# Kernel tuning notes

Measured on AMD Instinct MI355X. Metric: run time of the kernel, lower is better.

Reference implementation:

```python
import jax, jax.numpy as jnp
import numpy as np

TASK_WEIGHT = 1.0
PHYSICS_WEIGHT = 0.3
HZ = 50.0


def physics_scores(w, hz=HZ):
    """Vectorized port of _score_window_raw. w: [B, T, 3] float. Assumes T >= 20.
    Returns float32 [B] scores in {0, 55..90}."""
    w = jax.lax.stop_gradient(w)  # torch version detaches via .cpu().item()
    B, T, _ = w.shape
    n = T
    mean = jnp.mean(w, axis=1, keepdims=True)          # [B,1,3]
    d = w - mean                                        # centered
    tv = jnp.sum(d * d, axis=(1, 2)) / n                # [B] total (biased) variance
    reject = tv < 0.005
    # per-axis saturation check: too many samples pinned at max |value|
    absw = jnp.abs(w)                                   # [B,T,3]
    max_val = jnp.max(absw, axis=1)                     # [B,3]
    at_max_frac = jnp.mean(jnp.abs(absw - max_val[:, None, :]) < 0.01, axis=1)  # [B,3]
    reject |= jnp.any((max_val >= 0.5) & (at_max_frac > 0.2), axis=1)
    # jerk law (hz >= 50): central-difference twice, p95 of |jerk| pooled over axes
    if hz >= 50:
        dt = 1.0 / hz
        vel = (w[:, 2:, :] - w[:, :-2, :]) / (2 * dt)       # [B, T-2, 3]
        jerk = (vel[:, 2:, :] - vel[:, :-2, :]) / (2 * dt)  # [B, T-4, 3]
        jerks = jnp.abs(jerk).reshape(B, -1)                # [B, 3*(T-4)]
        js = jnp.sort(jerks, axis=1)
        p95_idx = int(jerks.shape[1] * 0.95)                # matches jerks[int(len*0.95)]
        reject |= js[:, p95_idx] > 5000
    # variance-tier score
    s1 = jnp.where(tv > 10.0, 90.0,
         jnp.where(tv > 2.0, 80.0,
         jnp.where(tv > 0.5, 70.0, 58.0)))
    # zero-crossing rate of centered x-axis
    dx = d[:, :, 0]                                      # [B,T]
    zcr = jnp.sum(dx[:, 1:] * dx[:, :-1] < 0, axis=1) / n
    s2 = jnp.where(zcr > 0.15, 85.0, jnp.where(zcr > 0.07, 70.0, 55.0))
    score = jnp.floor((s1 + s2) / 2.0)                   # int() truncation (values positive)
    return jnp.where(reject, 0.0, score).astype(jnp.float32)


def setup_inputs() -> dict:
    key = jax.random.key(0)
    k1, k2, k3 = jax.random.split(key, 3)
    B, T, C = 32768, 512, 128
    predictions = jax.random.normal(k1, (B, C), dtype=jnp.float32)
    labels = jax.random.randint(k2, (B,), 0, C, dtype=jnp.int64)
    # scale accel so physics checks pass with realistic-looking noise (std 0.1 m/s^2)
    imu_windows = 0.1 * jax.random.normal(k3, (B, T, 3), dtype=jnp.float32)
    return {"predictions": predictions, "labels": labels, "imu_windows": imu_windows}


def reference(predictions, labels, imu_windows):
    # task loss: mean cross-entropy
    logp = jax.nn.log_softmax(predictions, axis=-1)                      # [B,C]
    task_loss = -jnp.mean(jnp.take_along_axis(logp, labels[:, None], axis=1)[:, 0])
    # physics penalty
    scores = physics_scores(imu_windows, HZ)                             # [B]
    physics_penalty = jnp.mean(1.0 - scores / 100.0)
    return TASK_WEIGHT * task_loss + PHYSICS_WEIGHT * physics_penalty
```

## Files before the change

### kernel.cpp

```cpp
#include <hip/hip_runtime.h>
#include <math.h>

template <int CTRL>
__device__ __forceinline__ float dpp_zero_f(float x) {
    return __int_as_float(__builtin_amdgcn_update_dpp(
        0, __float_as_int(x), CTRL, 0xf, 0xf, true));
}
template <int CTRL>
__device__ __forceinline__ float dpp_self_f(float x) {
    return __int_as_float(__builtin_amdgcn_update_dpp(
        __float_as_int(x), __float_as_int(x), CTRL, 0xf, 0xf, false));
}
template <int CTRL>
__device__ __forceinline__ int dpp_zero_i(int x) {
    return __builtin_amdgcn_update_dpp(0, x, CTRL, 0xf, 0xf, true);
}

__device__ __forceinline__ float dpp_sum_f(float x) {
    x += dpp_zero_f<0x111>(x);
    x += dpp_zero_f<0x112>(x);
    x += dpp_zero_f<0x114>(x);
    x += dpp_zero_f<0x118>(x);
    x += dpp_zero_f<0x142>(x);
    x += dpp_zero_f<0x143>(x);
    return __int_as_float(__builtin_amdgcn_readlane(__float_as_int(x), 63));
}
__device__ __forceinline__ float dpp_max_f(float x) {
    x = fmaxf(x, dpp_self_f<0x111>(x));
    x = fmaxf(x, dpp_self_f<0x112>(x));
    x = fmaxf(x, dpp_self_f<0x114>(x));
    x = fmaxf(x, dpp_self_f<0x118>(x));
    x = fmaxf(x, dpp_self_f<0x142>(x));
    x = fmaxf(x, dpp_self_f<0x143>(x));
    return __int_as_float(__builtin_amdgcn_readlane(__float_as_int(x), 63));
}
__device__ __forceinline__ int dpp_sum_i(int x) {
    x += dpp_zero_i<0x111>(x);
    x += dpp_zero_i<0x112>(x);
    x += dpp_zero_i<0x114>(x);
    x += dpp_zero_i<0x118>(x);
    x += dpp_zero_i<0x142>(x);
    x += dpp_zero_i<0x143>(x);
    return __builtin_amdgcn_readlane(x, 63);
}

template <int CT_T, int CT_C>
__global__ void fused_kernel(const float* __restrict__ imu,
                             const float* __restrict__ preds,
                             const int* __restrict__ labels,
                             float* __restrict__ taskP,
                             float* __restrict__ scoreP,
                             int B, int T_rt, int C_rt) {
    extern __shared__ float lds[];
    __shared__ float shT[4], shS[4];
    const int wave = threadIdx.x >> 6, lane = threadIdx.x & 63;
    const int row = blockIdx.x * 4 + wave;
    const int T = (CT_T > 0) ? CT_T : T_rt;
    const int N = T * 3;
    float* L = lds + wave * N;
    const bool active = (row < B);

    if (active) {
        const float4* src4 = (const float4*)(imu + (size_t)row * (size_t)N);
        float4* dst4 = (float4*)L;
        const int n4 = N >> 2;
        for (int i = lane; i < n4; i += 64) dst4[i] = src4[i];
    }

    float loss = 0.f;
    if (active) {
        const int C = (CT_C > 0) ? CT_C : C_rt;
        constexpr int NV = (CT_C > 0) ? (CT_C / 64) : 16;
        const int nv = (CT_C > 0) ? NV : ((C_rt + 63) >> 6);
        const float* x = preds + (size_t)row * (size_t)C;
        float vals[NV];
        float m = -3.4e38f;
#pragma unroll
        for (int i = 0; i < NV; i++) {
            if (CT_C == 0 && i >= nv) break;
            const int c = lane + (i << 6);
            float v = (CT_C > 0 || c < C) ? x[c] : -3.4e38f;
            vals[i] = v;
            m = fmaxf(m, v);
        }
        m = dpp_max_f(m);
        float s = 0.f;
#pragma unroll
        for (int i = 0; i < NV; i++) {
            if (CT_C == 0 && i >= nv) break;
            const int c = lane + (i << 6);
            if (CT_C > 0 || c < C) s += expf(vals[i] - m);
        }
        s = dpp_sum_f(s);
        const int label = labels[row];
        const int src = label & 63, idx = label >> 6;
        float cand = vals[0];
#pragma unroll
        for (int i = 1; i < NV; i++) {
            if (CT_C == 0 && i >= nv) break;
            if (i == idx) cand = vals[i];
        }
        float xl = __shfl(cand, src, 64);
        loss = logf(s) + m - xl;
    }
    __syncthreads();

    float score = 0.f;
    if (active) {
        constexpr int KMAX = (CT_T > 0) ? (CT_T + 63) / 64 : 16;
        const int kmax = (CT_T > 0) ? KMAX : ((T_rt + 63) >> 6);
        float v0[KMAX], v1[KMAX], v2[KMAX];
        float sum0 = 0, sum1 = 0, sum2 = 0, sq = 0;
        float mx0 = 0, mx1 = 0, mx2 = 0;
        int jerkcnt = 0;
#pragma unroll
        for (int k = 0; k < KMAX; k++) {
            if (CT_T == 0 && k >= kmax) break;
            const int t = lane + (k << 6);
            float a = 0, b = 0, c = 0;
            if (CT_T > 0 || t < T) { a = L[t * 3 + 0]; b = L[t * 3 + 1]; c = L[t * 3 + 2]; }
            v0[k] = a; v1[k] = b; v2[k] = c;
            sum0 += a; sum1 += b; sum2 += c;
            sq += a * a + b * b + c * c;
            mx0 = fmaxf(mx0, fabsf(a));
            mx1 = fmaxf(mx1, fabsf(b));
            mx2 = fmaxf(mx2, fabsf(c));
            if (t < T - 4) {
                float a2 = L[(t + 2) * 3 + 0], b2 = L[(t + 2) * 3 + 1], c2 = L[(t + 2) * 3 + 2];
                float a4 = L[(t + 4) * 3 + 0], b4 = L[(t + 4) * 3 + 1], c4 = L[(t + 4) * 3 + 2];
                jerkcnt += (fabsf(625.f * (a4 - 2.f * a2 + a)) > 5000.f);
                jerkcnt += (fabsf(625.f * (b4 - 2.f * b2 + b)) > 5000.f);
                jerkcnt += (fabsf(625.f * (c4 - 2.f * c2 + c)) > 5000.f);
            }
        }
        sum0 = dpp_sum_f(sum0);
        sum1 = dpp_sum_f(sum1);
        sum2 = dpp_sum_f(sum2);
        sq   = dpp_sum_f(sq);
        mx0  = dpp_max_f(mx0);
        mx1  = dpp_max_f(mx1);
        mx2  = dpp_max_f(mx2);
        const float n = (float)T;
        const float m0 = sum0 / n;
        const float tv = (sq - (sum0 * sum0 + sum1 * sum1 + sum2 * sum2) / n) / n;

        int a0 = 0, a1 = 0, a2c = 0, zc = 0;
#pragma unroll
        for (int k = 0; k < KMAX; k++) {
            if (CT_T == 0 && k >= kmax) break;
            const int t = lane + (k << 6);
            if (CT_T > 0 || t < T) {
                a0  += (fabsf(fabsf(v0[k]) - mx0) < 0.01f);
                a1  += (fabsf(fabsf(v1[k]) - mx1) < 0.01f);
                a2c += (fabsf(fabsf(v2[k]) - mx2) < 0.01f);
                if (t < T - 1) {
                    float dxt = v0[k] - m0;
                    float dxn = L[(t + 1) * 3 + 0] - m0;
                    zc += (dxt * dxn < 0.f);
                }
            }
        }
        int pk1 = a0 | (a1 << 10) | (a2c << 20);
        int pk2 = zc | (jerkcnt << 16);
        pk1 = dpp_sum_i(pk1);
        pk2 = dpp_sum_i(pk2);
        a0 = pk1 & 1023; a1 = (pk1 >> 10) & 1023; a2c = (pk1 >> 20) & 1023;
        zc = pk2 & 0xffff; jerkcnt = pk2 >> 16;

        bool reject = (tv < 0.005f);
        const float fT = (float)T;
        if (mx0 >= 0.5f && (a0  / fT) > 0.2f) reject = true;
        if (mx1 >= 0.5f && (a1  / fT) > 0.2f) reject = true;
        if (mx2 >= 0.5f && (a2c / fT) > 0.2f) reject = true;
        const int jtot = (T - 4) * 3;
        const int p95 = (int)((double)jtot * 0.95);
        if (jerkcnt >= jtot - p95) reject = true;

        const float s1 = tv > 10.f ? 90.f : (tv > 2.f ? 80.f : (tv > 0.5f ? 70.f : 58.f));
        const float zcr = zc / fT;
        const float s2 = zcr > 0.15f ? 85.f : (zcr > 0.07f ? 70.f : 55.f);
        score = floorf((s1 + s2) * 0.5f);
        if (reject) score = 0.f;
    }

    if (lane == 0) { shT[wave] = loss; shS[wave] = score; }
    __syncthreads();
    if (threadIdx.x == 0) {
        taskP[blockIdx.x]  = shT[0] + shT[1] + shT[2] + shT[3];
        scoreP[blockIdx.x] = shS[0] + shS[1] + shS[2] + shS[3];
    }
}

__device__ __forceinline__ float wave_reduce_sum_shfl(float v) {
#pragma unroll
    for (int off = 32; off > 0; off >>= 1) v += __shfl_xor(v, off, 64);
    return v;
}

__global__ void finalize_kernel(const float* __restrict__ p1, const float* __restrict__ p2,
                                int n1, int n2, float* __restrict__ out, int B) {
    __shared__ float sh1[4], sh2[4];
    const int tid = threadIdx.x;
    float s1 = 0.f, s2 = 0.f;
    for (int i = tid; i < n1; i += 256) s1 += p1[i];
    for (int i = tid; i < n2; i += 256) s2 += p2[i];
    s1 = wave_reduce_sum_shfl(s1);
    s2 = wave_reduce_sum_shfl(s2);
    const int wave = tid >> 6, lane = tid & 63;
    if (lane == 0) { sh1[wave] = s1; sh2[wave] = s2; }
    __syncthreads();
    if (tid == 0) {
        float task = (sh1[0] + sh1[1] + sh1[2] + sh1[3]) / (float)B;
        float pen  = 1.f - (sh2[0] + sh2[1] + sh2[2] + sh2[3]) / (100.f * (float)B);
        out[0] = task + 0.3f * pen;
    }
}

extern "C" void kernel_launch(void* const* d_in, const int* in_sizes, int n_in,
                              void* d_out, int out_size, void* d_ws, size_t ws_size,
                              hipStream_t stream) {
    const float* preds = (const float*)d_in[0];
    const int* labels  = (const int*)d_in[1];
    const float* imu   = (const float*)d_in[2];
    float* out = (float*)d_out;

    const int B = in_sizes[1];
    const int C = in_sizes[0] / B;
    const int T = in_sizes[2] / (3 * B);

    const int blocks = (B + 3) / 4;
    float* p1 = (float*)d_ws;
    float* p2 = p1 + blocks;

    const size_t smem = (size_t)4 * (size_t)T * 3 * sizeof(float);
    if (T == 512 && C == 128)
        fused_kernel<512, 128><<<blocks, 256, smem, stream>>>(imu, preds, labels, p1, p2, B, T, C);
    else
        fused_kernel<0, 0><<<blocks, 256, smem, stream>>>(imu, preds, labels, p1, p2, B, T, C);

    finalize_kernel<<<1, 256, 0, stream>>>(p1, p2, blocks, blocks, out, B);
}
```

Measured before the change: 304.9 us.

## Load IMU window into registers per lane, dropping LDS staging

For the T=512, C=128 case, each lane now loads a contiguous chunk of 8 timesteps plus a 4-step halo straight from global memory into registers using float4 loads, and computes the stats, jerk and zero-crossing counts from registers. This removes the LDS staging, the block barrier and the strided LDS reads, and lets the kernel run with no dynamic shared memory. The cost is 36 floats of registers per lane and redundant halo loads that overlap neighbouring lanes, and the global load pattern becomes strided per lane (stride of 96 bytes). A separate generic kernel keeps the LDS path for other shapes.

```diff
diff --git a/kernel.cpp b/kernel.cpp
--- a/kernel.cpp
+++ b/kernel.cpp
@@ -44,93 +44,54 @@
     return __builtin_amdgcn_readlane(x, 63);
 }
 
-template <int CT_T, int CT_C>
-__global__ void fused_kernel(const float* __restrict__ imu,
-                             const float* __restrict__ preds,
-                             const int* __restrict__ labels,
-                             float* __restrict__ taskP,
-                             float* __restrict__ scoreP,
-                             int B, int T_rt, int C_rt) {
-    extern __shared__ float lds[];
+__global__ void fused_reg_kernel(const float* __restrict__ imu,
+                                 const float* __restrict__ preds,
+                                 const int* __restrict__ labels,
+                                 float* __restrict__ taskP,
+                                 float* __restrict__ scoreP, int B) {
+    constexpr int T = 512, C = 128, N = T * 3;
     __shared__ float shT[4], shS[4];
     const int wave = threadIdx.x >> 6, lane = threadIdx.x & 63;
     const int row = blockIdx.x * 4 + wave;
-    const int T = (CT_T > 0) ? CT_T : T_rt;
-    const int N = T * 3;
-    float* L = lds + wave * N;
-    const bool active = (row < B);
-
-    if (active) {
-        const float4* src4 = (const float4*)(imu + (size_t)row * (size_t)N);
-        float4* dst4 = (float4*)L;
-        const int n4 = N >> 2;
-        for (int i = lane; i < n4; i += 64) dst4[i] = src4[i];
-    }
-
-    float loss = 0.f;
-    if (active) {
-        const int C = (CT_C > 0) ? CT_C : C_rt;
-        constexpr int NV = (CT_C > 0) ? (CT_C / 64) : 16;
-        const int nv = (CT_C > 0) ? NV : ((C_rt + 63) >> 6);
-        const float* x = preds + (size_t)row * (size_t)C;
-        float vals[NV];
-        float m = -3.4e38f;
-#pragma unroll
-        for (int i = 0; i < NV; i++) {
-            if (CT_C == 0 && i >= nv) break;
-            const int c = lane + (i << 6);
-            float v = (CT_C > 0 || c < C) ? x[c] : -3.4e38f;
-            vals[i] = v;
-            m = fmaxf(m, v);
-        }
-        m = dpp_max_f(m);
-        float s = 0.f;
-#pragma unroll
-        for (int i = 0; i < NV; i++) {
-            if (CT_C == 0 && i >= nv) break;
-            const int c = lane + (i << 6);
-            if (CT_C > 0 || c < C) s += expf(vals[i] - m);
-        }
-        s = dpp_sum_f(s);
+    float loss = 0.f, score = 0.f;
+
+    if (row < B) {
+        const float* x = preds + (size_t)row * C;
+        const float c0 = x[lane], c1 = x[lane + 64];
+        const float m = dpp_max_f(fmaxf(c0, c1));
+        const float s = dpp_sum_f(expf(c0 - m) + expf(c1 - m));
         const int label = labels[row];
-        const int src = label & 63, idx = label >> 6;
-        float cand = vals[0];
-#pragma unroll
-        for (int i = 1; i < NV; i++) {
-            if (CT_C == 0 && i >= nv) break;
-            if (i == idx) cand = vals[i];
-        }
-        float xl = __shfl(cand, src, 64);
+        const float cand = ((label >> 6) == 0) ? c0 : c1;
+        const float xl = __shfl(cand, label & 63, 64);
         loss = logf(s) + m - xl;
-    }
-    __syncthreads();
-
-    float score = 0.f;
-    if (active) {
-        constexpr int KMAX = (CT_T > 0) ? (CT_T + 63) / 64 : 16;
-        const int kmax = (CT_T > 0) ? KMAX : ((T_rt + 63) >> 6);
-        float v0[KMAX], v1[KMAX], v2[KMAX];
+
+        const float* wr = imu + (size_t)row * N;
+        float f[36];
+#pragma unroll
+        for (int j = 0; j < 9; j++) {
+            int off = lane * 24 + j * 4;
+            if (off > N - 4) off = N - 4;
+            const float4 q = *(const float4*)(wr + off);
+            f[j * 4 + 0] = q.x; f[j * 4 + 1] = q.y;
+            f[j * 4 + 2] = q.z; f[j * 4 + 3] = q.w;
+        }
+
+        const int t0 = lane * 8;
         float sum0 = 0, sum1 = 0, sum2 = 0, sq = 0;
         float mx0 = 0, mx1 = 0, mx2 = 0;
         int jerkcnt = 0;
 #pragma unroll
-        for (int k = 0; k < KMAX; k++) {
-            if (CT_T == 0 && k >= kmax) break;
-            const int t = lane + (k << 6);
-            float a = 0, b = 0, c = 0;
-            if (CT_T > 0 || t < T) { a = L[t * 3 + 0]; b = L[t * 3 + 1]; c = L[t * 3 + 2]; }
-            v0[k] = a; v1[k] = b; v2[k] = c;
+        for (int j = 0; j < 8; j++) {
+            const float a = f[3 * j], b = f[3 * j + 1], c = f[3 * j + 2];
             sum0 += a; sum1 += b; sum2 += c;
-            sq += a * a + b * b + c * c;
+            sq = fmaf(a, a, fmaf(b, b, fmaf(c, c, sq)));
             mx0 = fmaxf(mx0, fabsf(a));
             mx1 = fmaxf(mx1, fabsf(b));
             mx2 = fmaxf(mx2, fabsf(c));
-            if (t < T - 4) {
-                float a2 = L[(t + 2) * 3 + 0], b2 = L[(t + 2) * 3 + 1], c2 = L[(t + 2) * 3 + 2];
-                float a4 = L[(t + 4) * 3 + 0], b4 = L[(t + 4) * 3 + 1], c4 = L[(t + 4) * 3 + 2];
-                jerkcnt += (fabsf(625.f * (a4 - 2.f * a2 + a)) > 5000.f);
-                jerkcnt += (fabsf(625.f * (b4 - 2.f * b2 + b)) > 5000.f);
-                jerkcnt += (fabsf(625.f * (c4 - 2.f * c2 + c)) > 5000.f);
+            if (t0 + j < T - 4) {
+                jerkcnt += (fabsf(625.f * (f[3*(j+4)+0] - 2.f * f[3*(j+2)+0] + a)) > 5000.f);
+                jerkcnt += (fabsf(625.f * (f[3*(j+4)+1] - 2.f * f[3*(j+2)+1] + b)) > 5000.f);
+                jerkcnt += (fabsf(625.f * (f[3*(j+4)+2] - 2.f * f[3*(j+2)+2] + c)) > 5000.f);
             }
         }
         sum0 = dpp_sum_f(sum0);
@@ -146,18 +107,14 @@
 
         int a0 = 0, a1 = 0, a2c = 0, zc = 0;
 #pragma unroll
-        for (int k = 0; k < KMAX; k++) {
-            if (CT_T == 0 && k >= kmax) break;
-            const int t = lane + (k << 6);
-            if (CT_T > 0 || t < T) {
-                a0  += (fabsf(fabsf(v0[k]) - mx0) < 0.01f);
-                a1  += (fabsf(fabsf(v1[k]) - mx1) < 0.01f);
-                a2c += (fabsf(fabsf(v2[k]) - mx2) < 0.01f);
-                if (t < T - 1) {
-                    float dxt = v0[k] - m0;
-                    float dxn = L[(t + 1) * 3 + 0] - m0;
-                    zc += (dxt * dxn < 0.f);
-                }
+        for (int j = 0; j < 8; j++) {
+            a0  += (fabsf(fabsf(f[3 * j + 0]) - mx0) < 0.01f);
+            a1  += (fabsf(fabsf(f[3 * j + 1]) - mx1) < 0.01f);
+            a2c += (fabsf(fabsf(f[3 * j + 2]) - mx2) < 0.01f);
+            if (t0 + j < T - 1) {
+                const float dxt = f[3 * j + 0] - m0;
+                const float dxn = f[3 * j + 3] - m0;
+                zc += (dxt * dxn < 0.f);
             }
         }
         int pk1 = a0 | (a1 << 10) | (a2c << 20);
@@ -183,6 +140,104 @@
         if (reject) score = 0.f;
     }
 
+    if (lane == 0) { shT[wave] = loss; shS[wave] = score; }
+    __syncthreads();
+    if (threadIdx.x == 0) {
+        taskP[blockIdx.x]  = shT[0] + shT[1] + shT[2] + shT[3];
+        scoreP[blockIdx.x] = shS[0] + shS[1] + shS[2] + shS[3];
+    }
+}
+
+__global__ void fused_generic_kernel(const float* __restrict__ imu,
+                                     const float* __restrict__ preds,
+                                     const int* __restrict__ labels,
+                                     float* __restrict__ taskP,
+                                     float* __restrict__ scoreP,
+                                     int B, int T, int C) {
+    extern __shared__ float lds[];
+    __shared__ float shT[4], shS[4];
+    const int wave = threadIdx.x >> 6, lane = threadIdx.x & 63;
+    const int row = blockIdx.x * 4 + wave;
+    const int N = T * 3;
+    float* L = lds + wave * N;
+    const bool active = (row < B);
+
+    if (active) {
+        const float4* src4 = (const float4*)(imu + (size_t)row * (size_t)N);
+        float4* dst4 = (float4*)L;
+        const int n4 = N >> 2;
+        for (int i = lane; i < n4; i += 64) dst4[i] = src4[i];
+    }
+    float loss = 0.f;
+    if (active) {
+        const float* x = preds + (size_t)row * (size_t)C;
+        float m = -3.4e38f;
+        for (int c = lane; c < C; c += 64) m = fmaxf(m, x[c]);
+        m = dpp_max_f(m);
+        float s = 0.f;
+        for (int c = lane; c < C; c += 64) s += expf(x[c] - m);
+        s = dpp_sum_f(s);
+        const int label = labels[row];
+        float xl = (lane == 0) ? x[label] : 0.f;
+        xl = __shfl(xl, 0, 64);
+        loss = logf(s) + m - xl;
+    }
+    __syncthreads();
+    float score = 0.f;
+    if (active) {
+        float sum0 = 0, sum1 = 0, sum2 = 0, sq = 0;
+        float mx0 = 0, mx1 = 0, mx2 = 0;
+        int jerkcnt = 0;
+        for (int t = lane; t < T; t += 64) {
+            float a = L[t * 3], b = L[t * 3 + 1], c = L[t * 3 + 2];
+            sum0 += a; sum1 += b; sum2 += c;
+            sq += a * a + b * b + c * c;
+            mx0 = fmaxf(mx0, fabsf(a));
+            mx1 = fmaxf(mx1, fabsf(b));
+            mx2 = fmaxf(mx2, fabsf(c));
+            if (t < T - 4) {
+                float a2 = L[(t+2)*3], b2 = L[(t+2)*3+1], c2 = L[(t+2)*3+2];
+                float a4 = L[(t+4)*3], b4 = L[(t+4)*3+1], c4 = L[(t+4)*3+2];
+                jerkcnt += (fabsf(625.f * (a4 - 2.f*a2 + a)) > 5000.f);
+                jerkcnt += (fabsf(625.f * (b4 - 2.f*b2 + b)) > 5000.f);
+                jerkcnt += (fabsf(625.f * (c4 - 2.f*c2 + c)) > 5000.f);
+            }
+        }
+        sum0 = dpp_sum_f(sum0); sum1 = dpp_sum_f(sum1); sum2 = dpp_sum_f(sum2);
+        sq = dpp_sum_f(sq);
+        mx0 = dpp_max_f(mx0); mx1 = dpp_max_f(mx1); mx2 = dpp_max_f(mx2);
+        const float n = (float)T;
+        const float m0 = sum0 / n;
+        const float tv = (sq - (sum0*sum0 + sum1*sum1 + sum2*sum2) / n) / n;
+        int a0 = 0, a1 = 0, a2c = 0, zc = 0;
+        for (int t = lane; t < T; t += 64) {
+            a0  += (fabsf(fabsf(L[t*3+0]) - mx0) < 0.01f);
+            a1  += (fabsf(fabsf(L[t*3+1]) - mx1) < 0.01f);
+            a2c += (fabsf(fabsf(L[t*3+2]) - mx2) < 0.01f);
+            if (t < T - 1) {
+                float dxt = L[t*3] - m0, dxn = L[(t+1)*3] - m0;
+                zc += (dxt * dxn < 0.f);
+            }
+        }
+        int pk1 = a0 | (a1 << 10) | (a2c << 20);
+        int pk2 = zc | (jerkcnt << 16);
+        pk1 = dpp_sum_i(pk1); pk2 = dpp_sum_i(pk2);
+        a0 = pk1 & 1023; a1 = (pk1 >> 10) & 1023; a2c = (pk1 >> 20) & 1023;
+        zc = pk2 & 0xffff; jerkcnt = pk2 >> 16;
+        bool reject = (tv < 0.005f);
+        const float fT = (float)T;
+        if (mx0 >= 0.5f && (a0  / fT) > 0.2f) reject = true;
+        if (mx1 >= 0.5f && (a1  / fT) > 0.2f) reject = true;
+        if (mx2 >= 0.5f && (a2c / fT) > 0.2f) reject = true;
+        const int jtot = (T - 4) * 3;
+        const int p95 = (int)((double)jtot * 0.95);
+        if (jerkcnt >= jtot - p95) reject = true;
+        const float s1 = tv > 10.f ? 90.f : (tv > 2.f ? 80.f : (tv > 0.5f ? 70.f : 58.f));
+        const float zcr = zc / fT;
+        const float s2 = zcr > 0.15f ? 85.f : (zcr > 0.07f ? 70.f : 55.f);
+        score = floorf((s1 + s2) * 0.5f);
+        if (reject) score = 0.f;
+    }
     if (lane == 0) { shT[wave] = loss; shS[wave] = score; }
     __syncthreads();
     if (threadIdx.x == 0) {
@@ -232,11 +287,11 @@
     float* p1 = (float*)d_ws;
     float* p2 = p1 + blocks;
 
-    const size_t smem = (size_t)4 * (size_t)T * 3 * sizeof(float);
-    if (T == 512 && C == 128)
-        fused_kernel<512, 128><<<blocks, 256, smem, stream>>>(imu, preds, labels, p1, p2, B, T, C);
-    else
-        fused_kernel<0, 0><<<blocks, 256, smem, stream>>>(imu, preds, labels, p1, p2, B, T, C);
-
+    if (T == 512 && C == 128) {
+        fused_reg_kernel<<<blocks, 256, 0, stream>>>(imu, preds, labels, p1, p2, B);
+    } else {
+        const size_t smem = (size_t)4 * (size_t)T * 3 * sizeof(float);
+        fused_generic_kernel<<<blocks, 256, smem, stream>>>(imu, preds, labels, p1, p2, B, T, C);
+    }
     finalize_kernel<<<1, 256, 0, stream>>>(p1, p2, blocks, blocks, out, B);
 }
```

New measurement: 297.7 us. 1.02x faster.
